# Optimization experiments

Measured on AMD Instinct MI355X. Metric: run time of the kernel, lower is better.

## Reference

```python
import jax, jax.numpy as jnp
import numpy as np

B, D, L, R, O = 32768, 128, 3, 64, 64
EPS = 1e-5


def setup_inputs() -> dict:
    key = jax.random.key(0)
    ks = jax.random.split(key, 5)
    s_in = 1.0 / np.sqrt(D)
    s_r = 1.0 / np.sqrt(R)
    return {
        "x": jax.random.normal(ks[0], (B, D, L), dtype=jnp.float32),
        "layer0": jax.random.uniform(ks[1], (D, R), minval=-s_in, maxval=s_in, dtype=jnp.float32),
        "core1": jax.random.uniform(ks[2], (R, D, R), minval=-s_in, maxval=s_in, dtype=jnp.float32),
        "core2": jax.random.uniform(ks[3], (R, D, R), minval=-s_in, maxval=s_in, dtype=jnp.float32),
        "last": jax.random.uniform(ks[4], (R, O), minval=-s_r, maxval=s_r, dtype=jnp.float32),
        "ln_w": jnp.ones((D, L), dtype=jnp.float32),
        "ln_b": jnp.zeros((D, L), dtype=jnp.float32),
    }


def reference(x, layer0, core1, core2, last, ln_w, ln_b):
    # LayerNorm over the last two dims [D, L] with affine params
    mu = jnp.mean(x, axis=(1, 2), keepdims=True)
    var = jnp.var(x, axis=(1, 2), keepdims=True)
    xn = (x - mu) * jax.lax.rsqrt(var + EPS) * ln_w + ln_b  # [B, D, L]

    # Tensor-train contraction chain. The original builds a khatri-rao
    # [B, R*D] per step then matmuls with the reshaped [R*D, R] core;
    # einsum 'br,bd,rds->bs' computes the identical contraction fused.
    temp = xn[:, :, 0] @ layer0  # [B, R]
    temp = jnp.einsum("br,bd,rds->bs", temp, xn[:, :, 1], core1)
    temp = jnp.einsum("br,bd,rds->bs", temp, xn[:, :, 2], core2)
    return temp @ last  # [B, O]
```

## Files before the change

kernel.cpp:

```cpp
#include <hip/hip_runtime.h>
#include <hip/hip_fp16.h>

typedef _Float16 f16;
typedef _Float16 f16x8 __attribute__((ext_vector_type(8)));
typedef float f32x16 __attribute__((ext_vector_type(16)));

#define SPLAT8(s) ((f16x8){(s),(s),(s),(s),(s),(s),(s),(s)})

#define TB 128
#define SLOT0_OFF 0
#define SLOT1_OFF 32768
#define T_OFF     65536
#define XN12_OFF  81920
#define SMEM_BYTES 148480
#define WS_CT1   0
#define WS_CT2   1048576
#define WS_L0T   2097152
#define WS_LASTT 2113536

#define WAITBAR0() asm volatile("s_waitcnt vmcnt(0)\n\ts_barrier" ::: "memory")

__device__ __forceinline__ void gload_lds16(const void* g, void* l) {
  __builtin_amdgcn_global_load_lds(
      (const __attribute__((address_space(1))) unsigned int*)g,
      (__attribute__((address_space(3))) unsigned int*)l, 16, 0, 0);
}

__device__ __forceinline__ void issue_chunk32(const unsigned char* g,
                                              unsigned char* l, int tid) {
  gload_lds16(g + tid * 16, l + tid * 16);
  gload_lds16(g + tid * 16 + 16384, l + tid * 16 + 16384);
}

__device__ __forceinline__ unsigned pack_h2(float a, float b) {
  return (unsigned)__half_as_ushort(__float2half(a)) |
         ((unsigned)__half_as_ushort(__float2half(b)) << 16);
}

__device__ __forceinline__ void reduce_T(unsigned char* smem, f32x16 a0, f32x16 a1,
                                         int p, int kh, int mh, int h, int scol) {
  float* scr = (float*)(smem + (kh ? SLOT1_OFF : SLOT0_OFF));
  __syncthreads();
  if (p == 0) {
#pragma unroll
    for (int j = 0; j < 16; ++j) {
      const int r0 = (j & 3) + 8 * (j >> 2) + 4 * h;
      const int row = mh * 64 + r0;
      scr[row * 64 + scol] = a0[j];
      scr[(row + 32) * 64 + scol] = a1[j];
    }
  }
  __syncthreads();
  if (p == 1) {
#pragma unroll
    for (int j = 0; j < 16; ++j) {
      const int r0 = (j & 3) + 8 * (j >> 2) + 4 * h;
      const int row = mh * 64 + r0;
      scr[row * 64 + scol] += a0[j];
      scr[(row + 32) * 64 + scol] += a1[j];
    }
  }
  __syncthreads();
  if (p == 0) {
    const float* s0 = (const float*)(smem + SLOT0_OFF);
    const float* s1 = (const float*)(smem + SLOT1_OFF);
#pragma unroll
    for (int j = 0; j < 16; ++j) {
      const int r0 = (j & 3) + 8 * (j >> 2) + 4 * h;
      const int row = mh * 64 + kh * 32 + r0;
      const float vsum = s0[row * 64 + scol] + s1[row * 64 + scol];
      *(__half*)(smem + T_OFF + row * 128 + ((2 * scol) ^ ((row & 7) << 4))) =
          __float2half(vsum);
    }
  }
  __syncthreads();
}

__global__ void __launch_bounds__(512) tt_prep(
    const float* __restrict__ layer0, const float* __restrict__ core1,
    const float* __restrict__ core2, const float* __restrict__ last,
    unsigned char* __restrict__ ws) {
  const int tid = blockIdx.x * 512 + threadIdx.x;
  if (tid < 524288) {
    const int which = tid >> 18;
    const int w = tid & 262143;
    const float* core = which ? core2 : core1;
    unsigned char* ct = ws + (which ? WS_CT2 : WS_CT1);
    const int j   = w & 3;
    const int lp  = (w >> 2) & 63;
    const int blk = w >> 8;
    const int kbL = blk & 1;
    const int kh  = (blk >> 1) & 1;
    const int sb  = (blk >> 2) & 1;
    const int d   = blk >> 3;
    const int hh  = lp & 1;
    const int l31 = lp >> 1;
    const int s   = sb * 32 + l31;
    const int r0  = kh * 32 + kbL * 16 + hh * 8 + 2 * j;
    const unsigned val = pack_h2(core[r0 * 8192 + d * 64 + s],
                                 core[(r0 + 1) * 8192 + d * 64 + s]);
    *(unsigned*)(ct + (size_t)w * 4) = val;
  } else if (tid < 528384) {
    const int w = tid - 524288;
    const int r = w >> 6, j = w & 63, d = 2 * j;
    const unsigned val = pack_h2(layer0[d * 64 + r], layer0[(d + 1) * 64 + r]);
    *(unsigned*)(ws + WS_L0T + r * 256 + 4 * j) = val;
  } else if (tid < 530432) {
    const int w = tid - 528384;
    const int o = w >> 5, j = w & 31, r = 2 * j;
    const unsigned val = pack_h2(last[r * 64 + o], last[(r + 1) * 64 + o]);
    *(unsigned*)(ws + WS_LASTT + o * 128 + 4 * j) = val;
  }
}

__global__ void __launch_bounds__(1024, 4) tt_fused(
    const float* __restrict__ x, const float* __restrict__ lnw,
    const float* __restrict__ lnb, const unsigned char* __restrict__ ws,
    float* __restrict__ out) {
  __shared__ alignas(16) unsigned char smem[SMEM_BYTES];
  const int tid = threadIdx.x;
  const int wid = tid >> 6;
  const int lane = tid & 63;
  const int l31 = lane & 31;
  const int h = lane >> 5;
  const int p  = wid & 1;
  const int kh = (wid >> 1) & 1;
  const int sb = (wid >> 2) & 1;
  const int mh = (wid >> 3) & 1;
  const int bg0 = blockIdx.x * TB;
  const int scol = sb * 32 + l31;
  const int lp16 = (l31 * 2 + h) * 16;
  const int swzA = (l31 & 7) << 4;

  {
    float wv[6], bv[6];
#pragma unroll
    for (int k = 0; k < 6; ++k) { wv[k] = lnw[lane + 64 * k]; bv[k] = lnb[lane + 64 * k]; }
#pragma unroll
    for (int rr = 0; rr < 8; ++rr) {
      const int row = wid * 8 + rr;
      const float* xrow = x + (size_t)(bg0 + row) * 384;
      float v[6];
#pragma unroll
      for (int k = 0; k < 6; ++k) v[k] = xrow[lane + 64 * k];
      float s = 0.f, ss = 0.f;
#pragma unroll
      for (int k = 0; k < 6; ++k) { s += v[k]; ss += v[k] * v[k]; }
#pragma unroll
      for (int m = 1; m < 64; m <<= 1) { s += __shfl_xor(s, m); ss += __shfl_xor(ss, m); }
      const float mu = s * (1.f / 384.f);
      const float var = ss * (1.f / 384.f) - mu * mu;
      const float rstd = rsqrtf(var + 1e-5f);
#pragma unroll
      for (int k = 0; k < 6; ++k) {
        const int i = lane + 64 * k;
        const int d = i / 3;
        const int sl = i - 3 * d;
        const float xv = (v[k] - mu) * rstd * wv[k] + bv[k];
        if (sl == 0) {
          *(__half*)(smem + SLOT0_OFF + row * 256 + ((2 * d) ^ ((row & 7) << 4))) =
              __float2half(xv);
        } else {
          *(__half*)(smem + XN12_OFF + d * 520 + 4 * row + 2 * (sl - 1)) =
              __float2half(xv);
        }
      }
    }
  }
  __syncthreads();

  f32x16 acc0, acc1;

#pragma unroll
  for (int i = 0; i < 16; ++i) { acc0[i] = 0.f; acc1[i] = 0.f; }
  {
    const unsigned char* l0t = ws + WS_L0T;
#pragma unroll
    for (int kbL = 0; kbL < 2; ++kbL) {
      const int cb = (((p << 1) | kh) * 2 + kbL) * 32 + h * 16;
      f16x8 bf = *(const f16x8*)(l0t + scol * 256 + cb);
      f16x8 a0 = *(const f16x8*)(smem + SLOT0_OFF + (mh * 64 + l31) * 256 + (cb ^ swzA));
      f16x8 a1 = *(const f16x8*)(smem + SLOT0_OFF + (mh * 64 + 32 + l31) * 256 + (cb ^ swzA));
      acc0 = __builtin_amdgcn_mfma_f32_32x32x16_f16(a0, bf, acc0, 0, 0, 0);
      acc1 = __builtin_amdgcn_mfma_f32_32x32x16_f16(a1, bf, acc1, 0, 0, 0);
    }
  }
  reduce_T(smem, acc0, acc1, p, kh, mh, h, scol);

  for (int st = 0; st < 2; ++st) {
    const unsigned char* ctg = ws + (st ? WS_CT2 : WS_CT1);

    issue_chunk32(ctg, smem + SLOT0_OFF, tid);

    f16x8 tp00, tp01, tp10, tp11;
    {
      const int rb0 = kh * 64 + h * 16;
      const int ra = (mh * 64 + l31) * 128;
      const int rb = (mh * 64 + 32 + l31) * 128;
      tp00 = *(const f16x8*)(smem + T_OFF + ra + (rb0 ^ swzA));
      tp01 = *(const f16x8*)(smem + T_OFF + ra + ((rb0 + 32) ^ swzA));
      tp10 = *(const f16x8*)(smem + T_OFF + rb + (rb0 ^ swzA));
      tp11 = *(const f16x8*)(smem + T_OFF + rb + ((rb0 + 32) ^ swzA));
    }

#pragma unroll
    for (int i = 0; i < 16; ++i) { acc0[i] = 0.f; acc1[i] = 0.f; }

    const unsigned char* bpS0 = smem + SLOT0_OFF + p * 8192 + sb * 4096 + kh * 2048 + lp16;
    const unsigned char* bpS1 = bpS0 + 32768;
    const unsigned char* xp = smem + XN12_OFF + p * 520 +
                              4 * (mh * 64 + l31) + 2 * st;

#pragma unroll 1
    for (int cg = 0; cg < 32; ++cg) {
      const f16 ea0 = *(const f16*)(xp);
      const f16 ea1 = *(const f16*)(xp + 128);
      const f16 eb0 = *(const f16*)(xp + 1040);
      const f16 eb1 = *(const f16*)(xp + 1168);
      xp += 2080;
      WAITBAR0();
      if (cg < 31)
        issue_chunk32(ctg + (cg + 1) * 32768,
                      smem + ((cg + 1) & 1) * 32768, tid);
      const unsigned char* bp = (cg & 1) ? bpS1 : bpS0;
      {
        f16x8 bf0 = *(const f16x8*)(bp);
        f16x8 bf1 = *(const f16x8*)(bp + 1024);
        const f16x8 e0 = SPLAT8(ea0);
        const f16x8 e1 = SPLAT8(ea1);
        acc0 = __builtin_amdgcn_mfma_f32_32x32x16_f16(tp00 * e0, bf0, acc0, 0, 0, 0);
        acc1 = __builtin_amdgcn_mfma_f32_32x32x16_f16(tp10 * e1, bf0, acc1, 0, 0, 0);
        acc0 = __builtin_amdgcn_mfma_f32_32x32x16_f16(tp01 * e0, bf1, acc0, 0, 0, 0);
        acc1 = __builtin_amdgcn_mfma_f32_32x32x16_f16(tp11 * e1, bf1, acc1, 0, 0, 0);
      }
      {
        f16x8 bf0 = *(const f16x8*)(bp + 16384);
        f16x8 bf1 = *(const f16x8*)(bp + 16384 + 1024);
        const f16x8 e0 = SPLAT8(eb0);
        const f16x8 e1 = SPLAT8(eb1);
        acc0 = __builtin_amdgcn_mfma_f32_32x32x16_f16(tp00 * e0, bf0, acc0, 0, 0, 0);
        acc1 = __builtin_amdgcn_mfma_f32_32x32x16_f16(tp10 * e1, bf0, acc1, 0, 0, 0);
        acc0 = __builtin_amdgcn_mfma_f32_32x32x16_f16(tp01 * e0, bf1, acc0, 0, 0, 0);
        acc1 = __builtin_amdgcn_mfma_f32_32x32x16_f16(tp11 * e1, bf1, acc1, 0, 0, 0);
      }
    }
    reduce_T(smem, acc0, acc1, p, kh, mh, h, scol);
  }

  if (p == 0) {
    f32x16 accd;
#pragma unroll
    for (int i = 0; i < 16; ++i) accd[i] = 0.f;
    const unsigned char* lastT = ws + WS_LASTT;
    const int rbase = mh * 64 + kh * 32;
#pragma unroll
    for (int kb = 0; kb < 4; ++kb) {
      const int cb = kb * 32 + h * 16;
      f16x8 bf = *(const f16x8*)(lastT + scol * 128 + cb);
      f16x8 af = *(const f16x8*)(smem + T_OFF + (rbase + l31) * 128 + (cb ^ swzA));
      accd = __builtin_amdgcn_mfma_f32_32x32x16_f16(af, bf, accd, 0, 0, 0);
    }
#pragma unroll
    for (int j = 0; j < 16; ++j) {
      const int r0 = (j & 3) + 8 * (j >> 2) + 4 * h;
      out[(size_t)(bg0 + rbase + r0) * 64 + scol] = accd[j];
    }
  }
}

extern "C" void kernel_launch(void* const* d_in, const int* in_sizes, int n_in,
                              void* d_out, int out_size, void* d_ws, size_t ws_size,
                              hipStream_t stream) {
  const float* x      = (const float*)d_in[0];
  const float* layer0 = (const float*)d_in[1];
  const float* core1  = (const float*)d_in[2];
  const float* core2  = (const float*)d_in[3];
  const float* last   = (const float*)d_in[4];
  const float* lnw    = (const float*)d_in[5];
  const float* lnb    = (const float*)d_in[6];
  unsigned char* ws   = (unsigned char*)d_ws;
  float* outp         = (float*)d_out;

  tt_prep<<<1036, 512, 0, stream>>>(layer0, core1, core2, last, ws);
  tt_fused<<<256, 1024, 0, stream>>>(x, lnw, lnb, ws, outp);
}
```

Baseline: 97.50 us.

## Replace block-wide core staging with per-wave private LDS ring buffers

Each wave now streams only the core-tensor fragments it consumes into its own private 4KB double-buffered LDS region, waiting only on its own vmcnt instead of a block-wide barrier per chunk. This removes the 32 s_barrier synchronisations per stage across 16 waves and lets waves progress independently. In exchange each wave issues its own global loads, and any core fragment shared by several waves is fetched multiple times, which raises global/L2 traffic. The loop becomes 64 iterations of half the work, with a sched_barrier placed to keep the loads ahead of the MFMAs.

```diff
diff --git a/kernel.cpp b/kernel.cpp
--- a/kernel.cpp
+++ b/kernel.cpp
@@ -8,6 +8,7 @@
 #define SPLAT8(s) ((f16x8){(s),(s),(s),(s),(s),(s),(s),(s)})
 
 #define TB 128
+#define RING_OFF  0
 #define SLOT0_OFF 0
 #define SLOT1_OFF 32768
 #define T_OFF     65536
@@ -18,18 +19,10 @@
 #define WS_L0T   2097152
 #define WS_LASTT 2113536
 
-#define WAITBAR0() asm volatile("s_waitcnt vmcnt(0)\n\ts_barrier" ::: "memory")
-
 __device__ __forceinline__ void gload_lds16(const void* g, void* l) {
   __builtin_amdgcn_global_load_lds(
       (const __attribute__((address_space(1))) unsigned int*)g,
       (__attribute__((address_space(3))) unsigned int*)l, 16, 0, 0);
-}
-
-__device__ __forceinline__ void issue_chunk32(const unsigned char* g,
-                                              unsigned char* l, int tid) {
-  gload_lds16(g + tid * 16, l + tid * 16);
-  gload_lds16(g + tid * 16 + 16384, l + tid * 16 + 16384);
 }
 
 __device__ __forceinline__ unsigned pack_h2(float a, float b) {
@@ -130,7 +123,9 @@
   const int bg0 = blockIdx.x * TB;
   const int scol = sb * 32 + l31;
   const int lp16 = (l31 * 2 + h) * 16;
+  const int lane16 = lane * 16;
   const int swzA = (l31 & 7) << 4;
+  unsigned char* priv = smem + RING_OFF + wid * 4096;
 
   {
     float wv[6], bv[6];
@@ -188,9 +183,14 @@
   reduce_T(smem, acc0, acc1, p, kh, mh, h, scol);
 
   for (int st = 0; st < 2; ++st) {
-    const unsigned char* ctg = ws + (st ? WS_CT2 : WS_CT1);
-
-    issue_chunk32(ctg, smem + SLOT0_OFF, tid);
+    const unsigned char* ctg = ws + (st ? WS_CT2 : WS_CT1) +
+                               sb * 4096 + kh * 2048 + lp16;
+
+    {
+      const unsigned char* g = ctg + p * 8192;
+      gload_lds16(g, priv);
+      gload_lds16(g + 1024, priv + 1024);
+    }
 
     f16x8 tp00, tp01, tp10, tp11;
     {
@@ -206,43 +206,33 @@
 #pragma unroll
     for (int i = 0; i < 16; ++i) { acc0[i] = 0.f; acc1[i] = 0.f; }
 
-    const unsigned char* bpS0 = smem + SLOT0_OFF + p * 8192 + sb * 4096 + kh * 2048 + lp16;
-    const unsigned char* bpS1 = bpS0 + 32768;
     const unsigned char* xp = smem + XN12_OFF + p * 520 +
                               4 * (mh * 64 + l31) + 2 * st;
 
 #pragma unroll 1
-    for (int cg = 0; cg < 32; ++cg) {
-      const f16 ea0 = *(const f16*)(xp);
-      const f16 ea1 = *(const f16*)(xp + 128);
-      const f16 eb0 = *(const f16*)(xp + 1040);
-      const f16 eb1 = *(const f16*)(xp + 1168);
-      xp += 2080;
-      WAITBAR0();
-      if (cg < 31)
-        issue_chunk32(ctg + (cg + 1) * 32768,
-                      smem + ((cg + 1) & 1) * 32768, tid);
-      const unsigned char* bp = (cg & 1) ? bpS1 : bpS0;
-      {
-        f16x8 bf0 = *(const f16x8*)(bp);
-        f16x8 bf1 = *(const f16x8*)(bp + 1024);
-        const f16x8 e0 = SPLAT8(ea0);
-        const f16x8 e1 = SPLAT8(ea1);
-        acc0 = __builtin_amdgcn_mfma_f32_32x32x16_f16(tp00 * e0, bf0, acc0, 0, 0, 0);
-        acc1 = __builtin_amdgcn_mfma_f32_32x32x16_f16(tp10 * e1, bf0, acc1, 0, 0, 0);
-        acc0 = __builtin_amdgcn_mfma_f32_32x32x16_f16(tp01 * e0, bf1, acc0, 0, 0, 0);
-        acc1 = __builtin_amdgcn_mfma_f32_32x32x16_f16(tp11 * e1, bf1, acc1, 0, 0, 0);
+    for (int cg = 0; cg < 64; ++cg) {
+      const f16 e0s = *(const f16*)(xp);
+      const f16 e1s = *(const f16*)(xp + 128);
+      xp += 1040;
+      if (cg < 63) {
+        const unsigned char* g = ctg + (2 * (cg + 1) + p) * 8192;
+        unsigned char* l = priv + ((cg + 1) & 1) * 2048;
+        gload_lds16(g, l);
+        gload_lds16(g + 1024, l + 1024);
+        asm volatile("s_waitcnt vmcnt(2)" ::: "memory");
+      } else {
+        asm volatile("s_waitcnt vmcnt(0)" ::: "memory");
       }
-      {
-        f16x8 bf0 = *(const f16x8*)(bp + 16384);
-        f16x8 bf1 = *(const f16x8*)(bp + 16384 + 1024);
-        const f16x8 e0 = SPLAT8(eb0);
-        const f16x8 e1 = SPLAT8(eb1);
-        acc0 = __builtin_amdgcn_mfma_f32_32x32x16_f16(tp00 * e0, bf0, acc0, 0, 0, 0);
-        acc1 = __builtin_amdgcn_mfma_f32_32x32x16_f16(tp10 * e1, bf0, acc1, 0, 0, 0);
-        acc0 = __builtin_amdgcn_mfma_f32_32x32x16_f16(tp01 * e0, bf1, acc0, 0, 0, 0);
-        acc1 = __builtin_amdgcn_mfma_f32_32x32x16_f16(tp11 * e1, bf1, acc1, 0, 0, 0);
-      }
+      __builtin_amdgcn_sched_barrier(0);
+      const unsigned char* bp = priv + (cg & 1) * 2048 + lane16;
+      f16x8 bf0 = *(const f16x8*)(bp);
+      f16x8 bf1 = *(const f16x8*)(bp + 1024);
+      const f16x8 e0 = SPLAT8(e0s);
+      const f16x8 e1 = SPLAT8(e1s);
+      acc0 = __builtin_amdgcn_mfma_f32_32x32x16_f16(tp00 * e0, bf0, acc0, 0, 0, 0);
+      acc1 = __builtin_amdgcn_mfma_f32_32x32x16_f16(tp10 * e1, bf0, acc1, 0, 0, 0);
+      acc0 = __builtin_amdgcn_mfma_f32_32x32x16_f16(tp01 * e0, bf1, acc0, 0, 0, 0);
+      acc1 = __builtin_amdgcn_mfma_f32_32x32x16_f16(tp11 * e1, bf1, acc1, 0, 0, 0);
     }
     reduce_T(smem, acc0, acc1, p, kh, mh, h, scol);
   }
```

New measurement: 106.6 us. 1.09x slower.
